# Performance work log

Measured on AMD Instinct MI355X. Metric: run time of the kernel, lower is better.

The kernel has to match this reference:

```python
import jax, jax.numpy as jnp
import numpy as np

H = 64  # hidden_dim
NV = 100000
NU = 100000
E = 500000

def _mlp(x, w1, b1, w2, b2):
    return jax.nn.relu(x @ w1 + b1) @ w2 + b2

def setup_inputs() -> dict:
    key = jax.random.key(0)
    ks = jax.random.split(key, 24)
    def lin(k, fin, fout):
        k1, k2 = jax.random.split(k)
        lim = 1.0 / np.sqrt(fin)
        w = jax.random.uniform(k1, (fin, fout), jnp.float32, -lim, lim)
        b = jax.random.uniform(k2, (fout,), jnp.float32, -lim, lim)
        return w, b
    a2u_w1, a2u_b1 = lin(ks[0], 3 * H, 2 * H)
    a2u_w2, a2u_b2 = lin(ks[1], 2 * H, H)
    u_w1, u_b1 = lin(ks[2], 2 * H, H)
    u_w2, u_b2 = lin(ks[3], H, H)
    u2a_w1, u2a_b1 = lin(ks[4], 3 * H, 2 * H)
    u2a_w2, u2a_b2 = lin(ks[5], 2 * H, H)
    a_w1, a_b1 = lin(ks[6], 2 * H, H)
    a_w2, a_b2 = lin(ks[7], H, H)
    h_v = jax.random.normal(ks[8], (NV, H), jnp.float32)
    h_u = jax.random.normal(ks[9], (NU, H), jnp.float32)
    e_feat = jax.random.normal(ks[10], (E, H), jnp.float32)
    ei0 = jax.random.randint(ks[11], (E,), 0, NV)
    ei1 = jax.random.randint(ks[12], (E,), 0, NU)
    edge_index = jnp.stack([ei0, ei1]).astype(jnp.int64)
    return {
        "h_v": h_v, "h_u": h_u, "e_feat": e_feat, "edge_index": edge_index, "S": 5,
        "a2u_w1": a2u_w1, "a2u_b1": a2u_b1, "a2u_w2": a2u_w2, "a2u_b2": a2u_b2,
        "u_w1": u_w1, "u_b1": u_b1, "u_w2": u_w2, "u_b2": u_b2,
        "u2a_w1": u2a_w1, "u2a_b1": u2a_b1, "u2a_w2": u2a_w2, "u2a_b2": u2a_b2,
        "a_w1": a_w1, "a_b1": a_b1, "a_w2": a_w2, "a_b2": a_b2,
    }

def reference(h_v, h_u, e_feat, edge_index, S,
              a2u_w1, a2u_b1, a2u_w2, a2u_b2,
              u_w1, u_b1, u_w2, u_b2,
              u2a_w1, u2a_b1, u2a_w2, u2a_b2,
              a_w1, a_b1, a_w2, a_b2):
    src, dst = edge_index[0], edge_index[1]
    # a -> u messages: gather, concat, MLP, scatter-add, normalize by S
    msg_a2u = _mlp(jnp.concatenate([h_v[src], h_u[dst], e_feat], axis=-1),
                   a2u_w1, a2u_b1, a2u_w2, a2u_b2)
    m_u = jax.ops.segment_sum(msg_a2u, dst, num_segments=h_u.shape[0]) / S
    h_u_out = _mlp(jnp.concatenate([h_u, m_u], axis=-1), u_w1, u_b1, u_w2, u_b2)
    # u -> a messages
    msg_u2a = _mlp(jnp.concatenate([h_u_out[dst], h_v[src], e_feat], axis=-1),
                   u2a_w1, u2a_b1, u2a_w2, u2a_b2)
    m_v = jax.ops.segment_sum(msg_u2a, src, num_segments=h_v.shape[0])
    deg = jax.ops.segment_sum(jnp.ones((src.shape[0],), h_v.dtype), src,
                              num_segments=h_v.shape[0])
    m_v = m_v / jnp.maximum(deg, 1.0)[:, None]
    h_v_out = _mlp(jnp.concatenate([h_v, m_v], axis=-1), a_w1, a_b1, a_w2, a_b2)
    return (h_v_out, h_u_out)
```

## Files before the change

### kernel.cpp

```cpp
#include <hip/hip_runtime.h>
#include <hip/hip_bf16.h>
#include <stdint.h>


typedef __attribute__((ext_vector_type(8))) short short8v;
typedef __attribute__((ext_vector_type(4))) float f32x4;

__device__ __forceinline__ ushort f2bf_rn(float f) {
    union { float f; unsigned int u; } v; v.f = f;
    unsigned int u = v.u;
    unsigned int r = u + 0x7fffu + ((u >> 16) & 1u);
    return (ushort)(r >> 16);
}
__device__ __forceinline__ float bf2f(ushort h) {
    union { unsigned int u; float f; } v; v.u = ((unsigned int)h) << 16;
    return v.f;
}

__device__ __forceinline__ void unpack2(unsigned int u, float& a, float& b) {
    union { unsigned int i; float f; } x, y;
    x.i = u << 16;
    y.i = u & 0xffff0000u;
    a = x.f; b = y.f;
}

__device__ __forceinline__ void load16bf(const __hip_bfloat16* __restrict__ p, float* xr) {
    const uint4* q = reinterpret_cast<const uint4*>(p);
    uint4 a = q[0];
    uint4 b = q[1];
    unpack2(a.x, xr[0], xr[1]);  unpack2(a.y, xr[2], xr[3]);
    unpack2(a.z, xr[4], xr[5]);  unpack2(a.w, xr[6], xr[7]);
    unpack2(b.x, xr[8], xr[9]);  unpack2(b.y, xr[10], xr[11]);
    unpack2(b.z, xr[12], xr[13]); unpack2(b.w, xr[14], xr[15]);
}

__device__ __forceinline__ void load16f(const float* __restrict__ p, float* xr) {
    const float4* q = reinterpret_cast<const float4*>(p);
#pragma unroll
    for (int i = 0; i < 4; ++i) {
        float4 v = q[i];
        xr[4*i+0] = v.x; xr[4*i+1] = v.y; xr[4*i+2] = v.z; xr[4*i+3] = v.w;
    }
}

__device__ __forceinline__ void load16(const void* base, size_t off, int isbf, float* xr) {
    if (isbf) load16bf((const __hip_bfloat16*)base + off, xr);
    else      load16f((const float*)base + off, xr);
}

__device__ __forceinline__ void ld8f(const float* __restrict__ p, float* t) {
    float4 a = *(const float4*)p;
    float4 b = *(const float4*)(p + 4);
    t[0]=a.x; t[1]=a.y; t[2]=a.z; t[3]=a.w;
    t[4]=b.x; t[5]=b.y; t[6]=b.z; t[7]=b.w;
}

__device__ __forceinline__ void cvt8(const float* __restrict__ t, short8v& hi, short8v& lo) {
#pragma unroll
    for (int j = 0; j < 8; ++j) {
        ushort h = f2bf_rn(t[j]);
        hi[j] = (short)h;
        lo[j] = (short)f2bf_rn(t[j] - bf2f(h));
    }
}

__global__ void detect_kernel(const unsigned int* __restrict__ hv, int* __restrict__ flag) {
    __shared__ int cnt;
    if (threadIdx.x == 0) cnt = 0;
    __syncthreads();
    unsigned int w = hv[threadIdx.x];
    int ef = (w >> 7) & 0xff;
    if (ef >= 100 && ef <= 140) atomicAdd(&cnt, 1);
    __syncthreads();
    if (threadIdx.x == 0) flag[0] = (cnt > 256) ? 1 : 0;
}

struct WArgs {
    const void* p[16];
    int off[16];
    int cnt[16];
};

__global__ void cvt_all(WArgs wa, float* __restrict__ wf, const int* __restrict__ gflag) {
    const int isbf = gflag[0];
    const int t = blockIdx.y;
    const int i = blockIdx.x * 256 + threadIdx.x;
    if (i >= wa.cnt[t]) return;
    wf[wa.off[t] + i] = isbf ? __bfloat162float(((const __hip_bfloat16*)wa.p[t])[i])
                             : ((const float*)wa.p[t])[i];
}

__global__ void pack_w1(const float* __restrict__ w1, ushort* __restrict__ hi, ushort* __restrict__ lo) {
    int i = blockIdx.x * 256 + threadIdx.x;
    if (i >= 8 * 6 * 64 * 8) return;
    int j = i & 7;
    int lane = (i >> 3) & 63;
    int t = i >> 9;
    int kt = t % 6, nt = t / 6;
    float w = w1[(kt * 32 + (lane >> 4) * 8 + j) * 128 + nt * 16 + (lane & 15)];
    ushort h = f2bf_rn(w);
    hi[i] = h;
    lo[i] = f2bf_rn(w - bf2f(h));
}

__global__ void pack_w2(const float* __restrict__ w2, ushort* __restrict__ hi, ushort* __restrict__ lo) {
    int i = blockIdx.x * 256 + threadIdx.x;
    if (i >= 4 * 4 * 64 * 8) return;
    int j = i & 7;
    int lane = (i >> 3) & 63;
    int t = i >> 9;
    int ot = t & 3, pair = t >> 2;
    float w = w2[(pair * 32 + (lane >> 4) * 8 + j) * 64 + ot * 16 + (lane & 15)];
    ushort h = f2bf_rn(w);
    hi[i] = h;
    lo[i] = f2bf_rn(w - bf2f(h));
}

__global__ void deg_kernel(const int* __restrict__ src, float* __restrict__ degv, int E) {
    int e = blockIdx.x * 256 + threadIdx.x;
    if (e < E) atomicAdd(&degv[src[e]], 1.0f);
}

template <int ISBF>
__global__ __launch_bounds__(64, 4)
void edge_mlp_mfma(const void* __restrict__ A_, const void* __restrict__ B_,
                   const void* __restrict__ E_,
                   const int* __restrict__ src_idx, const int* __restrict__ dst_idx,
                   const int* __restrict__ gflag,
                   const ushort* __restrict__ w1hi, const ushort* __restrict__ w1lo,
                   const ushort* __restrict__ w2hi, const ushort* __restrict__ w2lo,
                   const float* __restrict__ b1, const float* __restrict__ b2,
                   float* __restrict__ accum, int E, int ph3) {
    if (gflag[0] != ISBF) return;

    __shared__ ushort hb_hi[16][40];
    __shared__ ushort hb_lo[16][40];
    __shared__ float  smt[16][17];
    __shared__ int rowS[16], gA[16], gB[16];

    const int lane = threadIdx.x;
    const int base = blockIdx.x * 16;
    const int cnt = min(16, E - base);
    const int eloc = lane & 15;
    const int khalf = (lane >> 4) * 8;

    if (lane < 16) {
        int e = base + ((lane < cnt) ? lane : (cnt - 1));
        int s = src_idx[e], d = dst_idx[e];
        rowS[lane] = ph3 ? s : d;
        gA[lane]   = ph3 ? d : s;
        gB[lane]   = ph3 ? s : d;
    }
    __syncthreads();

    short8v ah[6];
    short8v al[6];
    {
        const int elc = (eloc < cnt) ? eloc : (cnt - 1);
        if (ISBF) {
            const ushort* ra = (const ushort*)A_ + (size_t)gA[elc] * 64;
            const ushort* rb = (const ushort*)B_ + (size_t)gB[elc] * 64;
            const ushort* re = (const ushort*)E_ + (size_t)(base + elc) * 64;
            ah[0] = *(const short8v*)(ra + khalf);
            ah[1] = *(const short8v*)(ra + 32 + khalf);
            ah[2] = *(const short8v*)(rb + khalf);
            ah[3] = *(const short8v*)(rb + 32 + khalf);
            ah[4] = *(const short8v*)(re + khalf);
            ah[5] = *(const short8v*)(re + 32 + khalf);
        } else {
            const float* ra = (const float*)A_ + (size_t)gA[elc] * 64;
            const float* rb = (const float*)B_ + (size_t)gB[elc] * 64;
            const float* re = (const float*)E_ + (size_t)(base + elc) * 64;
            float t[8];
            ld8f(ra + khalf, t);      cvt8(t, ah[0], al[0]);
            ld8f(ra + 32 + khalf, t); cvt8(t, ah[1], al[1]);
            ld8f(rb + khalf, t);      cvt8(t, ah[2], al[2]);
            ld8f(rb + 32 + khalf, t); cvt8(t, ah[3], al[3]);
            ld8f(re + khalf, t);      cvt8(t, ah[4], al[4]);
            ld8f(re + 32 + khalf, t); cvt8(t, ah[5], al[5]);
        }
    }

    f32x4 acc2[4];
#pragma unroll
    for (int ot = 0; ot < 4; ++ot)
#pragma unroll
        for (int r = 0; r < 4; ++r)
            acc2[ot][r] = b2[ot * 16 + (lane >> 4) * 4 + r];

#pragma unroll 1
    for (int pair = 0; pair < 4; ++pair) {
#pragma unroll
        for (int nt2 = 0; nt2 < 2; ++nt2) {
            const int nt = pair * 2 + nt2;
            const float bv = b1[nt * 16 + eloc];
            f32x4 c1;
            c1[0] = bv; c1[1] = bv; c1[2] = bv; c1[3] = bv;
#pragma unroll
            for (int kt = 0; kt < 6; ++kt) {
                const size_t wo = (((size_t)(nt * 6 + kt)) * 64 + lane) * 8;
                const short8v bh = *(const short8v*)(w1hi + wo);
                const short8v bl = *(const short8v*)(w1lo + wo);
                c1 = __builtin_amdgcn_mfma_f32_16x16x32_bf16(ah[kt], bh, c1, 0, 0, 0);
                c1 = __builtin_amdgcn_mfma_f32_16x16x32_bf16(ah[kt], bl, c1, 0, 0, 0);
                if (!ISBF)
                    c1 = __builtin_amdgcn_mfma_f32_16x16x32_bf16(al[kt], bh, c1, 0, 0, 0);
            }
#pragma unroll
            for (int r = 0; r < 4; ++r) {
                float v = fmaxf(c1[r], 0.0f);
                ushort h = f2bf_rn(v);
                ushort l = f2bf_rn(v - bf2f(h));
                const int er = (lane >> 4) * 4 + r;
                hb_hi[er][nt2 * 16 + eloc] = h;
                hb_lo[er][nt2 * 16 + eloc] = l;
            }
        }
        __syncthreads();
        {
            const short8v bh = *(const short8v*)(&hb_hi[eloc][khalf]);
            const short8v bl = *(const short8v*)(&hb_lo[eloc][khalf]);
#pragma unroll
            for (int ot = 0; ot < 4; ++ot) {
                const size_t wo = (((size_t)(pair * 4 + ot)) * 64 + lane) * 8;
                const short8v wh = *(const short8v*)(w2hi + wo);
                const short8v wl = *(const short8v*)(w2lo + wo);
                acc2[ot] = __builtin_amdgcn_mfma_f32_16x16x32_bf16(wh, bh, acc2[ot], 0, 0, 0);
                acc2[ot] = __builtin_amdgcn_mfma_f32_16x16x32_bf16(wh, bl, acc2[ot], 0, 0, 0);
                acc2[ot] = __builtin_amdgcn_mfma_f32_16x16x32_bf16(wl, bh, acc2[ot], 0, 0, 0);
            }
        }
        __syncthreads();
    }

#pragma unroll 1
    for (int ot = 0; ot < 4; ++ot) {
        __syncthreads();
#pragma unroll
        for (int r = 0; r < 4; ++r)
            smt[eloc][(lane >> 4) * 4 + r] = acc2[ot][r];
        __syncthreads();
#pragma unroll 1
        for (int i = 0; i < 16; i += 4) {
            const int e = i + (lane >> 4);
            if (e < cnt)
                atomicAdd(&accum[(size_t)rowS[e] * 64 + ot * 16 + eloc], smt[e][eloc]);
        }
    }
}

__global__ __launch_bounds__(256)
void node_mlp(const void* __restrict__ hin,
              const float* __restrict__ m,
              const float* __restrict__ degv,
              const int* __restrict__ Sptr,
              const int* __restrict__ gflag,
              const float* __restrict__ w1, const float* __restrict__ b1,
              const float* __restrict__ w2, const float* __restrict__ b2,
              void* __restrict__ out_f, void* __restrict__ out_b,
              int N, int ph4) {
    const int isbf = gflag[0];
    const int n = blockIdx.x * 256 + threadIdx.x;
    if (n >= N) return;
    const float scale = ph4 ? (1.0f / fmaxf(degv[n], 1.0f))
                            : (1.0f / (float)Sptr[0]);
    const size_t offH = (size_t)n * 64;
    const float* pm = m + offH;

    float h[64];
#pragma unroll
    for (int j = 0; j < 64; ++j) h[j] = b1[j];
#pragma unroll 1
    for (int kc = 0; kc < 8; ++kc) {
        float xr[16];
        if (kc < 4) {
            load16(hin, offH + kc * 16, isbf, xr);
        } else {
            load16f(pm + (kc - 4) * 16, xr);
#pragma unroll
            for (int k = 0; k < 16; ++k) xr[k] *= scale;
        }
#pragma unroll
        for (int k = 0; k < 16; ++k)
#pragma unroll
            for (int j = 0; j < 64; ++j)
                h[j] = fmaf(xr[k], w1[(kc * 16 + k) * 64 + j], h[j]);
    }
#pragma unroll
    for (int j = 0; j < 64; ++j) h[j] = fmaxf(h[j], 0.0f);

    float acc[64];
#pragma unroll
    for (int o = 0; o < 64; ++o) acc[o] = b2[o];
#pragma unroll
    for (int j = 0; j < 64; ++j)
#pragma unroll
        for (int o = 0; o < 64; ++o)
            acc[o] = fmaf(h[j], w2[j * 64 + o], acc[o]);

    if (isbf) {
        unsigned int ob[32];
#pragma unroll
        for (int i = 0; i < 32; ++i) {
            __hip_bfloat162 p2 = __float22bfloat162_rn(make_float2(acc[2 * i], acc[2 * i + 1]));
            ob[i] = *reinterpret_cast<unsigned int*>(&p2);
        }
        uint4* qo = reinterpret_cast<uint4*>((__hip_bfloat16*)out_b + offH);
#pragma unroll
        for (int i = 0; i < 8; ++i) qo[i] = make_uint4(ob[4*i], ob[4*i+1], ob[4*i+2], ob[4*i+3]);
    } else {
        float4* qf = reinterpret_cast<float4*>((float*)out_f + offH);
#pragma unroll
        for (int i = 0; i < 16; ++i) qf[i] = make_float4(acc[4*i], acc[4*i+1], acc[4*i+2], acc[4*i+3]);
    }
}

extern "C" void kernel_launch(void* const* d_in, const int* in_sizes, int n_in,
                              void* d_out, int out_size, void* d_ws, size_t ws_size,
                              hipStream_t stream) {
    const void* h_v    = d_in[0];
    const void* h_u    = d_in[1];
    const void* e_feat = d_in[2];
    const int* eidx = (const int*)d_in[3];
    const int* Sptr = (const int*)d_in[4];

    const int NV_ = in_sizes[0] / 64;
    const int NU_ = in_sizes[1] / 64;
    const int E_  = in_sizes[2] / 64;
    const int* src = eidx;
    const int* dst = eidx + E_;

    const int maxN = (NV_ > NU_) ? NV_ : NU_;
    int*   flag = (int*)d_ws;
    float* mbuf = (float*)((char*)d_ws + 64);
    float* degv = mbuf + (size_t)maxN * 64;
    float* wf   = degv + NV_;

    WArgs wa;
    int accum = 0;
    int maxCnt = 0;
    for (int i = 0; i < 16; ++i) {
        wa.p[i] = d_in[5 + i];
        wa.off[i] = accum;
        wa.cnt[i] = in_sizes[5 + i];
        accum += in_sizes[5 + i];
        if (in_sizes[5 + i] > maxCnt) maxCnt = in_sizes[5 + i];
    }

    const int W1P = 8 * 6 * 64 * 8;
    const int W2P = 4 * 4 * 64 * 8;
    ushort* pk = (ushort*)(wf + accum);
    ushort* p1w1hi = pk;
    ushort* p1w1lo = p1w1hi + W1P;
    ushort* p1w2hi = p1w1lo + W1P;
    ushort* p1w2lo = p1w2hi + W2P;
    ushort* p3w1hi = p1w2lo + W2P;
    ushort* p3w1lo = p3w1hi + W1P;
    ushort* p3w2hi = p3w1lo + W1P;
    ushort* p3w2lo = p3w2hi + W2P;

    detect_kernel<<<1, 512, 0, stream>>>((const unsigned int*)h_v, flag);

    dim3 cg((maxCnt + 255) / 256, 16);
    cvt_all<<<cg, 256, 0, stream>>>(wa, wf, flag);

    pack_w1<<<(W1P + 255) / 256, 256, 0, stream>>>(wf + wa.off[0], p1w1hi, p1w1lo);
    pack_w2<<<(W2P + 255) / 256, 256, 0, stream>>>(wf + wa.off[2], p1w2hi, p1w2lo);
    pack_w1<<<(W1P + 255) / 256, 256, 0, stream>>>(wf + wa.off[8], p3w1hi, p3w1lo);
    pack_w2<<<(W2P + 255) / 256, 256, 0, stream>>>(wf + wa.off[10], p3w2hi, p3w2lo);

    void* out_hv_f = d_out;
    void* out_hu_f = (void*)((float*)d_out + (size_t)NV_ * 64);
    void* out_hu_b = (void*)((__hip_bfloat16*)d_out + (size_t)NV_ * 64);

    hipMemsetAsync(mbuf, 0, (size_t)maxN * 64 * sizeof(float), stream);

    const int egrid16 = (E_ + 15) / 16;

    edge_mlp_mfma<0><<<egrid16, 64, 0, stream>>>(h_v, h_u, e_feat, src, dst, flag,
        p1w1hi, p1w1lo, p1w2hi, p1w2lo,
        wf + wa.off[1], wf + wa.off[3], mbuf, E_, 0);
    edge_mlp_mfma<1><<<egrid16, 64, 0, stream>>>(h_v, h_u, e_feat, src, dst, flag,
        p1w1hi, p1w1lo, p1w2hi, p1w2lo,
        wf + wa.off[1], wf + wa.off[3], mbuf, E_, 0);

    const int ngridU = (NU_ + 255) / 256;
    node_mlp<<<ngridU, 256, 0, stream>>>(h_u, mbuf, nullptr, Sptr, flag,
        wf + wa.off[4], wf + wa.off[5], wf + wa.off[6], wf + wa.off[7],
        out_hu_f, out_hu_b, NU_, 0);

    hipMemsetAsync(mbuf, 0, (size_t)maxN * 64 * sizeof(float), stream);
    hipMemsetAsync(degv, 0, (size_t)NV_ * sizeof(float), stream);

    deg_kernel<<<(E_ + 255) / 256, 256, 0, stream>>>(src, degv, E_);

    edge_mlp_mfma<0><<<egrid16, 64, 0, stream>>>(out_hu_f, h_v, e_feat, src, dst, flag,
        p3w1hi, p3w1lo, p3w2hi, p3w2lo,
        wf + wa.off[9], wf + wa.off[11], mbuf, E_, 1);
    edge_mlp_mfma<1><<<egrid16, 64, 0, stream>>>(out_hu_b, h_v, e_feat, src, dst, flag,
        p3w1hi, p3w1lo, p3w2hi, p3w2lo,
        wf + wa.off[9], wf + wa.off[11], mbuf, E_, 1);

    const int ngridV = (NV_ + 255) / 256;
    node_mlp<<<ngridV, 256, 0, stream>>>(h_v, mbuf, degv, Sptr, flag,
        wf + wa.off[12], wf + wa.off[13], wf + wa.off[14], wf + wa.off[15],
        out_hv_f, d_out, NV_, 1);
}
```

Baseline: 938.4 us.

## Stage packed MLP weights in LDS with persistent 8-wave edge blocks

```diff
diff --git a/kernel.cpp b/kernel.cpp
--- a/kernel.cpp
+++ b/kernel.cpp
@@ -5,6 +5,9 @@
 
 typedef __attribute__((ext_vector_type(8))) short short8v;
 typedef __attribute__((ext_vector_type(4))) float f32x4;
+
+#define WSYNC() do { asm volatile("s_waitcnt lgkmcnt(0)" ::: "memory"); \
+                     __builtin_amdgcn_sched_barrier(0); } while (0)
 
 __device__ __forceinline__ ushort f2bf_rn(float f) {
     union { float f; unsigned int u; } v; v.f = f;
@@ -122,7 +125,7 @@
 }
 
 template <int ISBF>
-__global__ __launch_bounds__(64, 4)
+__global__ __launch_bounds__(512, 1)
 void edge_mlp_mfma(const void* __restrict__ A_, const void* __restrict__ B_,
                    const void* __restrict__ E_,
                    const int* __restrict__ src_idx, const int* __restrict__ dst_idx,
@@ -133,118 +136,158 @@
                    float* __restrict__ accum, int E, int ph3) {
     if (gflag[0] != ISBF) return;
 
-    __shared__ ushort hb_hi[16][40];
-    __shared__ ushort hb_lo[16][40];
-    __shared__ float  smt[16][17];
-    __shared__ int rowS[16], gA[16], gB[16];
-
-    const int lane = threadIdx.x;
-    const int base = blockIdx.x * 16;
-    const int cnt = min(16, E - base);
+    __shared__ __align__(16) char smem[153088];
+    ushort* sw1h = (ushort*)smem;
+    ushort* sw1l = sw1h + 24576;
+    ushort* sw2h = sw1l + 24576;
+    ushort* sw2l = sw2h + 8192;
+    ushort* shb  = sw2l + 8192;
+    int*    sidx = (int*)(shb + 10240);
+
+    const int tid = threadIdx.x;
+    {
+        const uint4* g1h = (const uint4*)w1hi;
+        const uint4* g1l = (const uint4*)w1lo;
+        const uint4* g2h = (const uint4*)w2hi;
+        const uint4* g2l = (const uint4*)w2lo;
+        uint4* d1h = (uint4*)sw1h;
+        uint4* d1l = (uint4*)sw1l;
+        uint4* d2h = (uint4*)sw2h;
+        uint4* d2l = (uint4*)sw2l;
+        for (int i = tid; i < 3072; i += 512) d1h[i] = g1h[i];
+        for (int i = tid; i < 3072; i += 512) d1l[i] = g1l[i];
+        for (int i = tid; i < 1024; i += 512) d2h[i] = g2h[i];
+        for (int i = tid; i < 1024; i += 512) d2l[i] = g2l[i];
+    }
+    __syncthreads();
+
+    const int wid  = tid >> 6;
+    const int lane = tid & 63;
     const int eloc = lane & 15;
     const int khalf = (lane >> 4) * 8;
-
-    if (lane < 16) {
-        int e = base + ((lane < cnt) ? lane : (cnt - 1));
-        int s = src_idx[e], d = dst_idx[e];
-        rowS[lane] = ph3 ? s : d;
-        gA[lane]   = ph3 ? d : s;
-        gB[lane]   = ph3 ? s : d;
-    }
-    __syncthreads();
-
-    short8v ah[6];
-    short8v al[6];
-    {
-        const int elc = (eloc < cnt) ? eloc : (cnt - 1);
-        if (ISBF) {
-            const ushort* ra = (const ushort*)A_ + (size_t)gA[elc] * 64;
-            const ushort* rb = (const ushort*)B_ + (size_t)gB[elc] * 64;
-            const ushort* re = (const ushort*)E_ + (size_t)(base + elc) * 64;
-            ah[0] = *(const short8v*)(ra + khalf);
-            ah[1] = *(const short8v*)(ra + 32 + khalf);
-            ah[2] = *(const short8v*)(rb + khalf);
-            ah[3] = *(const short8v*)(rb + 32 + khalf);
-            ah[4] = *(const short8v*)(re + khalf);
-            ah[5] = *(const short8v*)(re + 32 + khalf);
-        } else {
-            const float* ra = (const float*)A_ + (size_t)gA[elc] * 64;
-            const float* rb = (const float*)B_ + (size_t)gB[elc] * 64;
-            const float* re = (const float*)E_ + (size_t)(base + elc) * 64;
-            float t[8];
-            ld8f(ra + khalf, t);      cvt8(t, ah[0], al[0]);
-            ld8f(ra + 32 + khalf, t); cvt8(t, ah[1], al[1]);
-            ld8f(rb + khalf, t);      cvt8(t, ah[2], al[2]);
-            ld8f(rb + 32 + khalf, t); cvt8(t, ah[3], al[3]);
-            ld8f(re + khalf, t);      cvt8(t, ah[4], al[4]);
-            ld8f(re + 32 + khalf, t); cvt8(t, ah[5], al[5]);
-        }
-    }
-
-    f32x4 acc2[4];
+    ushort* hw_hi = shb + wid * 1280;
+    ushort* hw_lo = hw_hi + 640;
+    float*  smt   = (float*)hw_hi;
+    int* rowS = sidx + wid * 48;
+    int* gA   = rowS + 16;
+    int* gB   = rowS + 32;
+
+    float b1v[8];
+    float b2r[4][4];
+#pragma unroll
+    for (int nt = 0; nt < 8; ++nt) b1v[nt] = b1[nt * 16 + eloc];
 #pragma unroll
     for (int ot = 0; ot < 4; ++ot)
 #pragma unroll
-        for (int r = 0; r < 4; ++r)
-            acc2[ot][r] = b2[ot * 16 + (lane >> 4) * 4 + r];
+        for (int r = 0; r < 4; ++r) b2r[ot][r] = b2[ot * 16 + (lane >> 4) * 4 + r];
+
+    const int ntile = (E + 127) >> 7;
+    for (int t = blockIdx.x; t < ntile; t += gridDim.x) {
+        const int ebase = t * 128 + wid * 16;
+        const int cnt = min(16, E - ebase);
+        if (cnt <= 0) continue;
+
+        if (lane < 16) {
+            int e = ebase + ((lane < cnt) ? lane : (cnt - 1));
+            int s = src_idx[e], d = dst_idx[e];
+            rowS[lane] = ph3 ? s : d;
+            gA[lane]   = ph3 ? d : s;
+            gB[lane]   = ph3 ? s : d;
+        }
+        WSYNC();
+
+        short8v ah[6], al[6];
+        {
+            const int elc = (eloc < cnt) ? eloc : (cnt - 1);
+            if (ISBF) {
+                const ushort* ra = (const ushort*)A_ + (size_t)gA[elc] * 64;
+                const ushort* rb = (const ushort*)B_ + (size_t)gB[elc] * 64;
+                const ushort* re = (const ushort*)E_ + (size_t)(ebase + elc) * 64;
+                ah[0] = *(const short8v*)(ra + khalf);
+                ah[1] = *(const short8v*)(ra + 32 + khalf);
+                ah[2] = *(const short8v*)(rb + khalf);
+                ah[3] = *(const short8v*)(rb + 32 + khalf);
+                ah[4] = *(const short8v*)(re + khalf);
+                ah[5] = *(const short8v*)(re + 32 + khalf);
+            } else {
+                const float* ra = (const float*)A_ + (size_t)gA[elc] * 64;
+                const float* rb = (const float*)B_ + (size_t)gB[elc] * 64;
+                const float* re = (const float*)E_ + (size_t)(ebase + elc) * 64;
+                float tt[8];
+                ld8f(ra + khalf, tt);      cvt8(tt, ah[0], al[0]);
+                ld8f(ra + 32 + khalf, tt); cvt8(tt, ah[1], al[1]);
+                ld8f(rb + khalf, tt);      cvt8(tt, ah[2], al[2]);
+                ld8f(rb + 32 + khalf, tt); cvt8(tt, ah[3], al[3]);
+                ld8f(re + khalf, tt);      cvt8(tt, ah[4], al[4]);
+                ld8f(re + 32 + khalf, tt); cvt8(tt, ah[5], al[5]);
+            }
+        }
+
+        f32x4 acc2[4];
+#pragma unroll
+        for (int ot = 0; ot < 4; ++ot)
+#pragma unroll
+            for (int r = 0; r < 4; ++r) acc2[ot][r] = b2r[ot][r];
 
 #pragma unroll 1
-    for (int pair = 0; pair < 4; ++pair) {
-#pragma unroll
-        for (int nt2 = 0; nt2 < 2; ++nt2) {
-            const int nt = pair * 2 + nt2;
-            const float bv = b1[nt * 16 + eloc];
-            f32x4 c1;
-            c1[0] = bv; c1[1] = bv; c1[2] = bv; c1[3] = bv;
-#pragma unroll
-            for (int kt = 0; kt < 6; ++kt) {
-                const size_t wo = (((size_t)(nt * 6 + kt)) * 64 + lane) * 8;
-                const short8v bh = *(const short8v*)(w1hi + wo);
-                const short8v bl = *(const short8v*)(w1lo + wo);
-                c1 = __builtin_amdgcn_mfma_f32_16x16x32_bf16(ah[kt], bh, c1, 0, 0, 0);
-                c1 = __builtin_amdgcn_mfma_f32_16x16x32_bf16(ah[kt], bl, c1, 0, 0, 0);
-                if (!ISBF)
-                    c1 = __builtin_amdgcn_mfma_f32_16x16x32_bf16(al[kt], bh, c1, 0, 0, 0);
+        for (int pair = 0; pair < 4; ++pair) {
+#pragma unroll
+            for (int nt2 = 0; nt2 < 2; ++nt2) {
+                const int nt = pair * 2 + nt2;
+                const float bv = b1v[nt];
+                f32x4 c1;
+                c1[0] = bv; c1[1] = bv; c1[2] = bv; c1[3] = bv;
+#pragma unroll
+                for (int kt = 0; kt < 6; ++kt) {
+                    const int wo = ((nt * 6 + kt) * 64 + lane) * 8;
+                    const short8v bh = *(const short8v*)(sw1h + wo);
+                    const short8v bl = *(const short8v*)(sw1l + wo);
+                    c1 = __builtin_amdgcn_mfma_f32_16x16x32_bf16(ah[kt], bh, c1, 0, 0, 0);
+                    c1 = __builtin_amdgcn_mfma_f32_16x16x32_bf16(ah[kt], bl, c1, 0, 0, 0);
+                    if (!ISBF)
+                        c1 = __builtin_amdgcn_mfma_f32_16x16x32_bf16(al[kt], bh, c1, 0, 0, 0);
+                }
+#pragma unroll
+                for (int r = 0; r < 4; ++r) {
+                    float v = fmaxf(c1[r], 0.0f);
+                    ushort h = f2bf_rn(v);
+                    ushort l = f2bf_rn(v - bf2f(h));
+                    const int er = (lane >> 4) * 4 + r;
+                    hw_hi[er * 40 + nt2 * 16 + eloc] = h;
+                    hw_lo[er * 40 + nt2 * 16 + eloc] = l;
+                }
             }
-#pragma unroll
-            for (int r = 0; r < 4; ++r) {
-                float v = fmaxf(c1[r], 0.0f);
-                ushort h = f2bf_rn(v);
-                ushort l = f2bf_rn(v - bf2f(h));
-                const int er = (lane >> 4) * 4 + r;
-                hb_hi[er][nt2 * 16 + eloc] = h;
-                hb_lo[er][nt2 * 16 + eloc] = l;
+            WSYNC();
+            {
+                const short8v bh = *(const short8v*)(hw_hi + eloc * 40 + khalf);
+                const short8v bl = *(const short8v*)(hw_lo + eloc * 40 + khalf);
+                WSYNC();
+#pragma unroll
+                for (int ot = 0; ot < 4; ++ot) {
+                    const int wo = ((pair * 4 + ot) * 64 + lane) * 8;
+                    const short8v wh = *(const short8v*)(sw2h + wo);
+                    const short8v wl = *(const short8v*)(sw2l + wo);
+                    acc2[ot] = __builtin_amdgcn_mfma_f32_16x16x32_bf16(wh, bh, acc2[ot], 0, 0, 0);
+                    acc2[ot] = __builtin_amdgcn_mfma_f32_16x16x32_bf16(wh, bl, acc2[ot], 0, 0, 0);
+                    acc2[ot] = __builtin_amdgcn_mfma_f32_16x16x32_bf16(wl, bh, acc2[ot], 0, 0, 0);
+                }
             }
         }
-        __syncthreads();
-        {
-            const short8v bh = *(const short8v*)(&hb_hi[eloc][khalf]);
-            const short8v bl = *(const short8v*)(&hb_lo[eloc][khalf]);
-#pragma unroll
-            for (int ot = 0; ot < 4; ++ot) {
-                const size_t wo = (((size_t)(pair * 4 + ot)) * 64 + lane) * 8;
-                const short8v wh = *(const short8v*)(w2hi + wo);
-                const short8v wl = *(const short8v*)(w2lo + wo);
-                acc2[ot] = __builtin_amdgcn_mfma_f32_16x16x32_bf16(wh, bh, acc2[ot], 0, 0, 0);
-                acc2[ot] = __builtin_amdgcn_mfma_f32_16x16x32_bf16(wh, bl, acc2[ot], 0, 0, 0);
-                acc2[ot] = __builtin_amdgcn_mfma_f32_16x16x32_bf16(wl, bh, acc2[ot], 0, 0, 0);
+
+#pragma unroll 1
+        for (int ot = 0; ot < 4; ++ot) {
+            WSYNC();
+#pragma unroll
+            for (int r = 0; r < 4; ++r)
+                smt[eloc * 17 + (lane >> 4) * 4 + r] = acc2[ot][r];
+            WSYNC();
+#pragma unroll 1
+            for (int i = 0; i < 16; i += 4) {
+                const int e = i + (lane >> 4);
+                if (e < cnt)
+                    atomicAdd(&accum[(size_t)rowS[e] * 64 + ot * 16 + eloc],
+                              smt[e * 17 + eloc]);
             }
-        }
-        __syncthreads();
-    }
-
-#pragma unroll 1
-    for (int ot = 0; ot < 4; ++ot) {
-        __syncthreads();
-#pragma unroll
-        for (int r = 0; r < 4; ++r)
-            smt[eloc][(lane >> 4) * 4 + r] = acc2[ot][r];
-        __syncthreads();
-#pragma unroll 1
-        for (int i = 0; i < 16; i += 4) {
-            const int e = i + (lane >> 4);
-            if (e < cnt)
-                atomicAdd(&accum[(size_t)rowS[e] * 64 + ot * 16 + eloc], smt[e][eloc]);
         }
     }
 }
@@ -375,12 +418,12 @@
 
     hipMemsetAsync(mbuf, 0, (size_t)maxN * 64 * sizeof(float), stream);
 
-    const int egrid16 = (E_ + 15) / 16;
-
-    edge_mlp_mfma<0><<<egrid16, 64, 0, stream>>>(h_v, h_u, e_feat, src, dst, flag,
+    const int EG = 256;
+
+    edge_mlp_mfma<0><<<EG, 512, 0, stream>>>(h_v, h_u, e_feat, src, dst, flag,
         p1w1hi, p1w1lo, p1w2hi, p1w2lo,
         wf + wa.off[1], wf + wa.off[3], mbuf, E_, 0);
-    edge_mlp_mfma<1><<<egrid16, 64, 0, stream>>>(h_v, h_u, e_feat, src, dst, flag,
+    edge_mlp_mfma<1><<<EG, 512, 0, stream>>>(h_v, h_u, e_feat, src, dst, flag,
         p1w1hi, p1w1lo, p1w2hi, p1w2lo,
         wf + wa.off[1], wf + wa.off[3], mbuf, E_, 0);
 
@@ -394,10 +437,10 @@
 
     deg_kernel<<<(E_ + 255) / 256, 256, 0, stream>>>(src, degv, E_);
 
-    edge_mlp_mfma<0><<<egrid16, 64, 0, stream>>>(out_hu_f, h_v, e_feat, src, dst, flag,
+    edge_mlp_mfma<0><<<EG, 512, 0, stream>>>(out_hu_f, h_v, e_feat, src, dst, flag,
         p3w1hi, p3w1lo, p3w2hi, p3w2lo,
         wf + wa.off[9], wf + wa.off[11], mbuf, E_, 1);
-    edge_mlp_mfma<1><<<egrid16, 64, 0, stream>>>(out_hu_b, h_v, e_feat, src, dst, flag,
+    edge_mlp_mfma<1><<<EG, 512, 0, stream>>>(out_hu_b, h_v, e_feat, src, dst, flag,
         p3w1hi, p3w1lo, p3w2hi, p3w2lo,
         wf + wa.off[9], wf + wa.off[11], mbuf, E_, 1);
 
```

New measurement: 767.8 us. 1.22x faster.
